# Kernel optimization log

Hardware: AMD Instinct MI355X
Metric: run time of the kernel (lower is better)

Reference implementation:

```python
import jax, jax.numpy as jnp
import numpy as np

B, S, D, H, L, DFF, NA = 128, 52, 1024, 16, 8, 4096, 1000
DK = D // H
KTOP = int((1.0 - 0.9) * S)  # per-row top-k kept before threshold = 5
EPS = 1e-5
SCALE = 1.0 / np.sqrt(DK).astype(np.float32)


def setup_inputs() -> dict:
    key = jax.random.key(0)
    ks = jax.random.split(key, 30)
    # token grid: channels 0,1 in [0,50) so only designated positions match special tokens
    x = jax.random.randint(ks[0], (B, S, 3), 0, 50).astype(jnp.int32)
    act = jax.random.randint(ks[1], (B, S), 0, NA).astype(jnp.int32)
    x = x.at[..., 2].set(act)
    x = x.at[:, 0].set(jnp.array([100, 0, 1], jnp.int32))    # SOS
    x = x.at[:, 26].set(jnp.array([100, 0, 2], jnp.int32))   # SEP
    x = x.at[:, 48:].set(jnp.array([100, 0, 0], jnp.int32))  # PAD tail

    def n(k, shape, scale=0.02):
        return (jax.random.normal(k, shape) * scale).astype(jnp.float32)

    return dict(
        x=x,
        action_emb=n(ks[2], (NA, D), 1.0),
        sep_token=n(ks[3], (D,), 1.0),
        bn_gamma=jnp.ones((S,), jnp.float32),
        bn_beta=jnp.zeros((S,), jnp.float32),
        Wq=n(ks[4], (L, D, D)), bq=jnp.zeros((L, D), jnp.float32),
        Wk=n(ks[5], (L, D, D)), bk=jnp.zeros((L, D), jnp.float32),
        Wv=n(ks[6], (L, D, D)), bv=jnp.zeros((L, D), jnp.float32),
        Wo=n(ks[7], (L, D, D)), bo=jnp.zeros((L, D), jnp.float32),
        W1=n(ks[8], (L, DFF, D)), b1=jnp.zeros((L, DFF), jnp.float32),
        W2=n(ks[9], (L, D, DFF)), b2=jnp.zeros((L, D), jnp.float32),
        ln1_g=jnp.ones((L, D), jnp.float32), ln1_b=jnp.zeros((L, D), jnp.float32),
        ln2_g=jnp.ones((L, D), jnp.float32), ln2_b=jnp.zeros((L, D), jnp.float32),
        Wout=n(ks[10], (3, D)), bout=jnp.zeros((3,), jnp.float32),
    )


def _ln(x, g, b):
    m = x.mean(-1, keepdims=True)
    v = x.var(-1, keepdims=True)
    return (x - m) * jax.lax.rsqrt(v + EPS) * g + b


def reference(x, action_emb, sep_token, bn_gamma, bn_beta,
              Wq, bq, Wk, bk, Wv, bv, Wo, bo,
              W1, b1, W2, b2, ln1_g, ln1_b, ln2_g, ln2_b, Wout, bout):
    PAD = jnp.array([100, 0, 0], x.dtype)
    SEP = jnp.array([100, 0, 2], x.dtype)
    pad = jnp.all(x == PAD, -1)            # [B,S]
    sep = jnp.all(x == SEP, -1)            # [B,S]
    valid = ~pad                            # attend only to non-pad keys

    # token-scatter embedding: sep positions -> sep_token, everything else -> action embedding
    h = jnp.where(sep[..., None], sep_token, action_emb[x[..., 2]])  # [B,S,D]

    # BatchNorm1d(52) over seq-as-channel dim (training-mode batch stats)
    mu = h.mean((0, 2), keepdims=True)
    var = h.var((0, 2), keepdims=True)
    h = (h - mu) * jax.lax.rsqrt(var + EPS) * bn_gamma[None, :, None] + bn_beta[None, :, None]

    for l in range(L):
        q = (h @ Wq[l].T + bq[l]).reshape(B, S, H, DK).transpose(0, 2, 1, 3)
        k = (h @ Wk[l].T + bk[l]).reshape(B, S, H, DK).transpose(0, 2, 1, 3)
        v = (h @ Wv[l].T + bv[l]).reshape(B, S, H, DK).transpose(0, 2, 1, 3)
        scores = jnp.einsum('bhqd,bhkd->bhqk', q, k) * SCALE       # [B,H,S,S]
        scores = jnp.where(valid[:, None, None, :], scores, -1e9)
        thr = jax.lax.top_k(scores, KTOP)[0][..., -1:]              # per-row k-th largest
        sparse = scores * (scores >= thr).astype(scores.dtype)      # zero out sub-threshold
        attn = jax.nn.softmax(sparse, axis=-1)
        o = jnp.einsum('bhqk,bhkd->bhqd', attn, v).transpose(0, 2, 1, 3).reshape(B, S, D)
        o = o @ Wo[l].T + bo[l]
        h = _ln(h + o, ln1_g[l], ln1_b[l])
        f = jax.nn.relu(h @ W1[l].T + b1[l]) @ W2[l].T + b2[l]
        h = _ln(h + f, ln2_g[l], ln2_b[l])

    y = h @ Wout.T + bout                                           # [B,S,3]
    return y[:, -1]
```

## Files before the change

kernel.cpp:

```cpp
#include <hip/hip_runtime.h>
#include <cstddef>
#include <cstdint>

#define B_    128
#define S_    52
#define D_    1024
#define H_    16
#define L_    8
#define DFF_  4096
#define DK_   64
#define T_    (B_*S_)
#define EPS_  1e-5f
#define SCALE_ 0.125f

typedef unsigned short ushortx4 __attribute__((ext_vector_type(4)));
typedef short  bf16x8 __attribute__((ext_vector_type(8)));
typedef float  f32x4  __attribute__((ext_vector_type(4)));

__device__ __forceinline__ unsigned short f2b(float f) {
  unsigned int u = __builtin_bit_cast(unsigned int, f);
  u = u + 0x7fffu + ((u >> 16) & 1u);
  return (unsigned short)(u >> 16);
}
__device__ __forceinline__ float b2f(unsigned short b) {
  unsigned int u = ((unsigned int)b) << 16;
  return __builtin_bit_cast(float, u);
}
__device__ __forceinline__ void gload16(const void* g, void* l) {
  __builtin_amdgcn_global_load_lds((const __attribute__((address_space(1))) unsigned int*)g,
      (__attribute__((address_space(3))) unsigned int*)l, 16, 0, 0);
}

__global__ __launch_bounds__(256) void k_embed(const int* __restrict__ x,
    const float* __restrict__ aemb, const float* __restrict__ sept,
    float* __restrict__ h, float* __restrict__ part, int* __restrict__ mask)
{
  int row = blockIdx.x;
  int b = row / S_;
  int s = row - b * S_;
  const int* xr = x + (size_t)row * 3;
  int x0 = xr[0], x1 = xr[1], x2 = xr[2];
  bool issep = (x0 == 100) && (x1 == 0) && (x2 == 2);
  bool ispad = (x0 == 100) && (x1 == 0) && (x2 == 0);
  int t = threadIdx.x;
  if (t == 0) mask[row] = ispad ? 0 : 1;
  const float* src = issep ? sept : (aemb + (size_t)x2 * D_);
  size_t base = (size_t)row * D_;
  float s1 = 0.f, s2 = 0.f;
#pragma unroll
  for (int i = 0; i < 4; ++i) {
    int d = t + i * 256;
    float v = src[d];
    h[base + d] = v;
    s1 += v;
    s2 += v * v;
  }
#pragma unroll
  for (int off = 32; off; off >>= 1) {
    s1 += __shfl_down(s1, off);
    s2 += __shfl_down(s2, off);
  }
  __shared__ float red[8];
  int lane = t & 63, wid = t >> 6;
  if (lane == 0) { red[wid] = s1; red[4 + wid] = s2; }
  __syncthreads();
  if (t == 0) {
    part[(size_t)s * B_ + b]        = red[0] + red[1] + red[2] + red[3];
    part[(size_t)(S_ + s) * B_ + b] = red[4] + red[5] + red[6] + red[7];
  }
}

__global__ __launch_bounds__(128) void k_bn_reduce(const float* __restrict__ part,
                                                   float* __restrict__ stats)
{
  int s = blockIdx.x;
  int t = threadIdx.x;
  float s1 = part[(size_t)s * B_ + t];
  float s2 = part[(size_t)(S_ + s) * B_ + t];
#pragma unroll
  for (int off = 32; off; off >>= 1) {
    s1 += __shfl_down(s1, off);
    s2 += __shfl_down(s2, off);
  }
  __shared__ float red[4];
  int lane = t & 63, wid = t >> 6;
  if (lane == 0) { red[wid] = s1; red[2 + wid] = s2; }
  __syncthreads();
  if (t == 0) {
    stats[s]      = red[0] + red[1];
    stats[S_ + s] = red[2] + red[3];
  }
}

__global__ __launch_bounds__(256) void k_bn_apply(float* __restrict__ h,
    const float* __restrict__ stats, const float* __restrict__ g,
    const float* __restrict__ bb, unsigned short* __restrict__ hb)
{
  int row = blockIdx.x;
  int s = row % S_;
  const float cnt = (float)(B_ * D_);
  float mu  = stats[s] / cnt;
  float var = stats[S_ + s] / cnt - mu * mu;
  float sc  = rsqrtf(var + EPS_) * g[s];
  float off = bb[s] - mu * sc;
  size_t base = (size_t)row * D_;
  int t = threadIdx.x;
#pragma unroll
  for (int i = 0; i < 4; ++i) {
    int d = t + i * 256;
    float v = h[base + d] * sc + off;
    h[base + d] = v;
    hb[base + d] = f2b(v);
  }
}

__global__ __launch_bounds__(256) void k_wconv(
    const float* __restrict__ wq, const float* __restrict__ wk,
    const float* __restrict__ wv, const float* __restrict__ wo,
    const float* __restrict__ w1, const float* __restrict__ w2,
    unsigned short* __restrict__ out)
{
  const size_t DD = (size_t)D_ * D_;
  const size_t DF = (size_t)DFF_ * D_;
  const size_t total = 4 * DD + 2 * DF;
  size_t stride = (size_t)gridDim.x * 256 * 4;
  for (size_t i = ((size_t)blockIdx.x * 256 + threadIdx.x) * 4; i < total; i += stride) {
    const float* src; size_t off;
    if      (i < DD)          { src = wq; off = i; }
    else if (i < 2 * DD)      { src = wk; off = i - DD; }
    else if (i < 3 * DD)      { src = wv; off = i - 2 * DD; }
    else if (i < 4 * DD)      { src = wo; off = i - 3 * DD; }
    else if (i < 4 * DD + DF) { src = w1; off = i - 4 * DD; }
    else                      { src = w2; off = i - 4 * DD - DF; }
    float4 v = *reinterpret_cast<const float4*>(src + off);
    ushortx4 o = { f2b(v.x), f2b(v.y), f2b(v.z), f2b(v.w) };
    *reinterpret_cast<ushortx4*>(out + i) = o;
  }
}

__global__ __launch_bounds__(256) void k_bcat(const float* __restrict__ bq,
    const float* __restrict__ bk, const float* __restrict__ bv,
    float* __restrict__ out)
{
  int i = blockIdx.x * 256 + threadIdx.x;
  int l = i / 3072, j = i - l * 3072;
  float v = (j < D_) ? bq[l * D_ + j] : (j < 2 * D_) ? bk[l * D_ + j - D_]
                                                     : bv[l * D_ + j - 2 * D_];
  out[i] = v;
}

__global__ void k_zero32(int* __restrict__ cnt) { cnt[threadIdx.x] = 0; }

template<int RELU, int OUTBF16>
__global__ __launch_bounds__(512, 4) void k_gemm_p(
    const unsigned short* __restrict__ A, const unsigned short* __restrict__ Wt,
    const float* __restrict__ bias, void* __restrict__ C0, void* __restrict__ C1,
    int Mtiles, int Ntiles, int parts, int K, int ldc, int* __restrict__ cnt)
{
  __shared__ unsigned short lds[3 * 12288];
  __shared__ int sTile;
  const int tid = threadIdx.x;
  const int w = tid >> 6, l = tid & 63;

  const int tpp = Mtiles * Ntiles;
  const int nwg = tpp * parts;
  const int KH = K / parts;
  const int NT = KH >> 5;

  const int colsw = 16 * ((l & 3) ^ ((l >> 3) & 3));
  const size_t r16 = (size_t)16 * K * 2;
  unsigned short* lA = lds + w * 1024;
  unsigned short* lB = lds + 8192 + w * 512;
  const int fr = l & 15, kg = l >> 4;
  const int wr = w >> 1, wc = w & 1;
  const int xk = 16 * (kg ^ ((fr >> 1) & 3));
  const int aOff = (wr * 64 + fr) * 64 + xk;
  const int bOff = 16384 + (wc * 64 + fr) * 64 + xk;

  for (;;) {
    if (tid == 0) sTile = atomicAdd(cnt, 1);
    __syncthreads();
    const int tl = sTile;
    if (tl >= nwg) break;
    const int part = tl / tpp;
    const int rem  = tl - part * tpp;
    const int bxn  = rem % Ntiles;
    const int bym  = rem / Ntiles;
    const int bm = bym * 256, bn = bxn * 128;

    const char* gA = (const char*)A + ((size_t)(bm + w * 32 + (l >> 2)) * K + (size_t)part * KH) * 2 + colsw;
    const char* gB = (const char*)Wt + ((size_t)(bn + w * 16 + (l >> 2)) * K + (size_t)part * KH) * 2 + colsw;

#define STAGE(tt, bb) do {                          \
    size_t ko_ = (size_t)(tt) * 64;                 \
    unsigned short* la_ = lA + (bb) * 12288;        \
    unsigned short* lb_ = lB + (bb) * 12288;        \
    gload16(gA + ko_,       la_);                   \
    gload16(gA + ko_ + r16, la_ + 512);             \
    gload16(gB + ko_,       lb_);                   \
  } while (0)

    f32x4 acc[4][4] = {};
    STAGE(0, 0);
    STAGE(1, 1);
    int cur = 0;
    for (int t = 0; t < NT; ++t) {
      if (t + 1 < NT) { asm volatile("s_waitcnt vmcnt(3)" ::: "memory"); }
      else            { asm volatile("s_waitcnt vmcnt(0)" ::: "memory"); }
      __builtin_amdgcn_sched_barrier(0);
      __builtin_amdgcn_s_barrier();
      __builtin_amdgcn_sched_barrier(0);
      if (t + 2 < NT) {
        int nb = cur + 2; if (nb >= 3) nb -= 3;
        STAGE(t + 2, nb);
      }
      const char* bp = (const char*)lds + cur * 24576;
      bf16x8 af[4], bfv[4];
#pragma unroll
      for (int mf = 0; mf < 4; ++mf)
        af[mf] = *(const bf16x8*)(bp + aOff + mf * 1024);
#pragma unroll
      for (int nf = 0; nf < 4; ++nf)
        bfv[nf] = *(const bf16x8*)(bp + bOff + nf * 1024);
      asm volatile("s_waitcnt lgkmcnt(0)" ::: "memory");
      __builtin_amdgcn_sched_barrier(0);
      __builtin_amdgcn_s_setprio(1);
#pragma unroll
      for (int mf = 0; mf < 4; ++mf)
#pragma unroll
        for (int nf = 0; nf < 4; ++nf)
          acc[mf][nf] = __builtin_amdgcn_mfma_f32_16x16x32_bf16(af[mf], bfv[nf], acc[mf][nf], 0, 0, 0);
      __builtin_amdgcn_s_setprio(0);
      __builtin_amdgcn_sched_barrier(0);
      cur = (cur == 2) ? 0 : cur + 1;
    }
#undef STAGE

    void* C = part ? C1 : C0;
#pragma unroll
    for (int nf = 0; nf < 4; ++nf) {
      int col = bn + wc * 64 + nf * 16 + fr;
      float bv = (part == 0) ? bias[col] : 0.f;
#pragma unroll
      for (int mf = 0; mf < 4; ++mf) {
        int row0 = bm + wr * 64 + mf * 16 + kg * 4;
#pragma unroll
        for (int j = 0; j < 4; ++j) {
          float v = acc[mf][nf][j] + bv;
          if (RELU) v = fmaxf(v, 0.f);
          if (OUTBF16)
            ((unsigned short*)C)[(size_t)(row0 + j) * ldc + col] = f2b(v);
          else
            ((float*)C)[(size_t)(row0 + j) * ldc + col] = v;
        }
      }
    }
  }
}

__global__ __launch_bounds__(64) void k_attn(const unsigned short* __restrict__ qkv,
    const int* __restrict__ mask, unsigned short* __restrict__ ao)
{
  __shared__ float sc[64][68];
  __shared__ unsigned short ph[64][68];
  __shared__ unsigned short plo[64][68];
  __shared__ unsigned short vT[64][68];
  __shared__ float dnm[64];

  int blk = blockIdx.x;
  int b = blk >> 4, hh = blk & 15;
  int l = threadIdx.x;
  int cl = l & 15, kg = l >> 4;
  const unsigned short* base = qkv + (size_t)(b * S_) * 3072 + hh * 64;

  {
    const unsigned short* vp = base + 2048 + l;
#pragma unroll 4
    for (int k = 0; k < S_; ++k)
      vT[l][k] = vp[(size_t)k * 3072];
#pragma unroll
    for (int k = S_; k < 64; ++k) vT[l][k] = 0;
  }

  bf16x8 qa[4][2], kb[4][2];
#pragma unroll
  for (int mi = 0; mi < 4; ++mi) {
    int row = mi * 16 + cl;
    bool ok = (row < S_);
    const unsigned short* qp = base + (size_t)row * 3072 + kg * 8;
#pragma unroll
    for (int ks = 0; ks < 2; ++ks) {
      bf16x8 z = {};
      qa[mi][ks] = ok ? *reinterpret_cast<const bf16x8*>(qp + ks * 32) : z;
      kb[mi][ks] = ok ? *reinterpret_cast<const bf16x8*>(qp + 1024 + ks * 32) : z;
    }
  }

  f32x4 acc[4][4] = {};
#pragma unroll
  for (int ks = 0; ks < 2; ++ks)
#pragma unroll
    for (int mi = 0; mi < 4; ++mi)
#pragma unroll
      for (int ci = 0; ci < 4; ++ci)
        acc[mi][ci] = __builtin_amdgcn_mfma_f32_16x16x32_bf16(qa[mi][ks], kb[ci][ks], acc[mi][ci], 0, 0, 0);

  int vld[4];
#pragma unroll
  for (int ci = 0; ci < 4; ++ci) {
    int col = ci * 16 + cl;
    vld[ci] = (col < S_) ? mask[b * S_ + col] : 0;
  }
#pragma unroll
  for (int mi = 0; mi < 4; ++mi)
#pragma unroll
    for (int ci = 0; ci < 4; ++ci)
#pragma unroll
      for (int j = 0; j < 4; ++j)
        sc[mi * 16 + kg * 4 + j][ci * 16 + cl] = vld[ci] ? acc[mi][ci][j] * SCALE_ : -1e9f;

  __syncthreads();

  if (l < S_) {
    float v0 = -3e38f, v1 = -3e38f, v2 = -3e38f, v3 = -3e38f, v4 = -3e38f;
    const float4* rp = reinterpret_cast<const float4*>(&sc[l][0]);
#pragma unroll
    for (int c4 = 0; c4 < 13; ++c4) {
      float4 x = rp[c4];
      float xs[4] = { x.x, x.y, x.z, x.w };
#pragma unroll
      for (int u = 0; u < 4; ++u) {
        float xv = xs[u];
        if      (xv > v0) { v4 = v3; v3 = v2; v2 = v1; v1 = v0; v0 = xv; }
        else if (xv > v1) { v4 = v3; v3 = v2; v2 = v1; v1 = xv; }
        else if (xv > v2) { v4 = v3; v3 = v2; v2 = xv; }
        else if (xv > v3) { v4 = v3; v3 = xv; }
        else if (xv > v4) { v4 = xv; }
      }
    }
    float thr = v4;
    float m = fmaxf(v0, 0.f);
    float denom = 0.f;
    for (int c = 0; c < S_; ++c) {
      float xv = sc[l][c];
      float sp = (xv >= thr) ? xv : 0.f;
      float e = __expf(sp - m);
      denom += e;
      unsigned short hi = f2b(e);
      ph[l][c] = hi;
      plo[l][c] = f2b(e - b2f(hi));
    }
#pragma unroll
    for (int c = S_; c < 64; ++c) { ph[l][c] = 0; plo[l][c] = 0; }
    dnm[l] = 1.f / denom;
  }
  __syncthreads();

  f32x4 o[4][4] = {};
#pragma unroll
  for (int ks = 0; ks < 2; ++ks) {
    bf16x8 vf[4];
#pragma unroll
    for (int di = 0; di < 4; ++di)
      vf[di] = *reinterpret_cast<const bf16x8*>(&vT[di * 16 + cl][ks * 32 + kg * 8]);
#pragma unroll
    for (int mi = 0; mi < 4; ++mi) {
      bf16x8 ahi = *reinterpret_cast<const bf16x8*>(&ph[mi * 16 + cl][ks * 32 + kg * 8]);
      bf16x8 alo = *reinterpret_cast<const bf16x8*>(&plo[mi * 16 + cl][ks * 32 + kg * 8]);
#pragma unroll
      for (int di = 0; di < 4; ++di) {
        o[mi][di] = __builtin_amdgcn_mfma_f32_16x16x32_bf16(ahi, vf[di], o[mi][di], 0, 0, 0);
        o[mi][di] = __builtin_amdgcn_mfma_f32_16x16x32_bf16(alo, vf[di], o[mi][di], 0, 0, 0);
      }
    }
  }

#pragma unroll
  for (int mi = 0; mi < 4; ++mi) {
    int row = mi * 16 + kg * 4;
    if (row < S_) {
#pragma unroll
      for (int j = 0; j < 4; ++j) {
        int r = row + j;
        float inv = dnm[r];
        unsigned short* aop = ao + (size_t)(b * S_ + r) * D_ + hh * DK_;
#pragma unroll
        for (int di = 0; di < 4; ++di)
          aop[di * 16 + cl] = f2b(o[mi][di][j] * inv);
      }
    }
  }
}

__global__ __launch_bounds__(256) void k_add_ln(float* __restrict__ h,
    const float* __restrict__ r0, const float* __restrict__ r1,
    const float* __restrict__ g, const float* __restrict__ bb,
    unsigned short* __restrict__ hb)
{
  int row = blockIdx.x;
  size_t base = (size_t)row * D_;
  int t = threadIdx.x;
  float xs[4];
  float s1 = 0.f, s2 = 0.f;
#pragma unroll
  for (int i = 0; i < 4; ++i) {
    int d = t + i * 256;
    float xv = h[base + d] + r0[base + d] + r1[base + d];
    xs[i] = xv;
    s1 += xv;
    s2 += xv * xv;
  }
#pragma unroll
  for (int off = 32; off; off >>= 1) {
    s1 += __shfl_down(s1, off);
    s2 += __shfl_down(s2, off);
  }
  __shared__ float red[8];
  int lane = t & 63, wid = t >> 6;
  if (lane == 0) { red[wid] = s1; red[4 + wid] = s2; }
  __syncthreads();
  if (t == 0) {
    red[0] = red[0] + red[1] + red[2] + red[3];
    red[4] = red[4] + red[5] + red[6] + red[7];
  }
  __syncthreads();
  float mean = red[0] / (float)D_;
  float var  = red[4] / (float)D_ - mean * mean;
  float inv  = rsqrtf(var + EPS_);
#pragma unroll
  for (int i = 0; i < 4; ++i) {
    int d = t + i * 256;
    float v = (xs[i] - mean) * inv * g[d] + bb[d];
    h[base + d] = v;
    hb[base + d] = f2b(v);
  }
}

__global__ __launch_bounds__(256) void k_final(const float* __restrict__ h,
    const float* __restrict__ Wout, const float* __restrict__ bout,
    float* __restrict__ y)
{
  int b = blockIdx.x;
  const float* hr = h + (size_t)(b * S_ + (S_ - 1)) * D_;
  int t = threadIdx.x;
  float p0 = 0.f, p1 = 0.f, p2 = 0.f;
  for (int d = t; d < D_; d += 256) {
    float xv = hr[d];
    p0 += xv * Wout[d];
    p1 += xv * Wout[D_ + d];
    p2 += xv * Wout[2 * D_ + d];
  }
#pragma unroll
  for (int off = 32; off; off >>= 1) {
    p0 += __shfl_down(p0, off);
    p1 += __shfl_down(p1, off);
    p2 += __shfl_down(p2, off);
  }
  __shared__ float red[12];
  int lane = t & 63, wid = t >> 6;
  if (lane == 0) { red[wid] = p0; red[4 + wid] = p1; red[8 + wid] = p2; }
  __syncthreads();
  if (t == 0) {
    y[b * 3 + 0] = red[0] + red[1] + red[2]  + red[3]  + bout[0];
    y[b * 3 + 1] = red[4] + red[5] + red[6]  + red[7]  + bout[1];
    y[b * 3 + 2] = red[8] + red[9] + red[10] + red[11] + bout[2];
  }
}

extern "C" void kernel_launch(void* const* d_in, const int* in_sizes, int n_in,
                              void* d_out, int out_size, void* d_ws, size_t ws_size,
                              hipStream_t stream)
{
  const int*   x    = (const int*)d_in[0];
  const float* aemb = (const float*)d_in[1];
  const float* sept = (const float*)d_in[2];
  const float* bng  = (const float*)d_in[3];
  const float* bnb  = (const float*)d_in[4];
  const float* Wq = (const float*)d_in[5];  const float* bq = (const float*)d_in[6];
  const float* Wk = (const float*)d_in[7];  const float* bk = (const float*)d_in[8];
  const float* Wv = (const float*)d_in[9];  const float* bv = (const float*)d_in[10];
  const float* Wo = (const float*)d_in[11]; const float* bo = (const float*)d_in[12];
  const float* W1 = (const float*)d_in[13]; const float* b1 = (const float*)d_in[14];
  const float* W2 = (const float*)d_in[15]; const float* b2 = (const float*)d_in[16];
  const float* ln1g = (const float*)d_in[17]; const float* ln1b = (const float*)d_in[18];
  const float* ln2g = (const float*)d_in[19]; const float* ln2b = (const float*)d_in[20];
  const float* Wout = (const float*)d_in[21]; const float* bout = (const float*)d_in[22];
  float* out = (float*)d_out;

  float* ws = (float*)d_ws;
  const size_t TD = (size_t)T_ * D_;
  const size_t DD = (size_t)D_ * D_;
  const size_t DF = (size_t)DFF_ * D_;
  float* h   = ws;
  float* tmp = ws + TD;
  unsigned short* hb   = (unsigned short*)(ws + 2 * TD);
  unsigned short* qkvb = (unsigned short*)(ws + 2 * TD + TD / 2);
  unsigned short* aob  = (unsigned short*)(ws + 4 * TD);
  unsigned short* ffb  = (unsigned short*)(ws + 4 * TD + TD / 2);
  unsigned short* wbuf = (unsigned short*)(ws + 6 * TD + TD / 2);
  float* Pff = ws + 4 * TD + TD / 2;
  float* Pqk = ws + 2 * TD + TD / 2;
  float* bqkv = ws + 6 * TD + TD / 2 + (4 * DD + 2 * DF) / 2;
  float* stats = bqkv + L_ * 3072;
  float* part  = stats + 2 * S_;
  int*   mask  = (int*)(part + 2 * S_ * B_);
  int*   cnt   = mask + T_;

  k_zero32<<<1, 32, 0, stream>>>(cnt);
  k_embed<<<T_, 256, 0, stream>>>(x, aemb, sept, h, part, mask);
  k_bn_reduce<<<S_, 128, 0, stream>>>(part, stats);
  k_bn_apply<<<T_, 256, 0, stream>>>(h, stats, bng, bnb, hb);
  k_bcat<<<(L_ * 3072) / 256, 256, 0, stream>>>(bq, bk, bv, bqkv);

  for (int l = 0; l < L_; ++l) {
    k_wconv<<<3072, 256, 0, stream>>>(Wq + l * DD, Wk + l * DD, Wv + l * DD,
                                      Wo + l * DD, W1 + l * DF, W2 + l * DF, wbuf);
    k_gemm_p<0, 1><<<512, 512, 0, stream>>>(hb, wbuf, bqkv + l * 3072,
        qkvb, qkvb, 26, 24, 1, 1024, 3072, cnt + l * 4 + 0);
    k_attn<<<B_ * H_, 64, 0, stream>>>(qkvb, mask, aob);
    k_gemm_p<0, 0><<<416, 512, 0, stream>>>(aob, wbuf + 3 * DD, bo + l * D_,
        tmp, Pff, 26, 8, 2, 1024, 1024, cnt + l * 4 + 1);
    k_add_ln<<<T_, 256, 0, stream>>>(h, tmp, Pff, ln1g + l * D_, ln1b + l * D_, hb);
    k_gemm_p<1, 1><<<512, 512, 0, stream>>>(hb, wbuf + 4 * DD, b1 + l * DFF_,
        ffb, ffb, 26, 32, 1, 1024, 4096, cnt + l * 4 + 2);
    k_gemm_p<0, 0><<<416, 512, 0, stream>>>(ffb, wbuf + 4 * DD + DF, b2 + l * D_,
        tmp, Pqk, 26, 8, 2, 4096, 1024, cnt + l * 4 + 3);
    k_add_ln<<<T_, 256, 0, stream>>>(h, tmp, Pqk, ln2g + l * D_, ln2b + l * D_, hb);
  }
  k_final<<<B_, 256, 0, stream>>>(h, Wout, bout, out);
}
```

Before: 2.771 ms.

## Replace persistent atomic-scheduled GEMM with 128x128 tiles and half-stage pipeline

Replaces the persistent GEMM, which fetched 256x128 tiles through an atomic counter with 512 threads, with a one-tile-per-block 128x128 kernel using 256 threads and an XCD-style block-index swizzle. The K loop now streams each K-step in two half-stages across a 5-slot LDS ring and splits the MFMA work into two halves with a barrier between them, so loads overlap more finely with compute. The counter-zeroing kernel and atomics go away. In exchange each block does less work, there are more launches' worth of blocks and more barriers per K-step, and the B tile gets reloaded more often.

Measured after the change: 2.765 ms. Within noise of the previous version (-0.2%).

```diff
diff --git a/kernel.cpp b/kernel.cpp
--- a/kernel.cpp
+++ b/kernel.cpp
@@ -149,110 +149,117 @@
   out[i] = v;
 }
 
-__global__ void k_zero32(int* __restrict__ cnt) { cnt[threadIdx.x] = 0; }
-
 template<int RELU, int OUTBF16>
-__global__ __launch_bounds__(512, 4) void k_gemm_p(
+__global__ __launch_bounds__(256, 4) void k_gemm5(
     const unsigned short* __restrict__ A, const unsigned short* __restrict__ Wt,
     const float* __restrict__ bias, void* __restrict__ C0, void* __restrict__ C1,
-    int Mtiles, int Ntiles, int parts, int K, int ldc, int* __restrict__ cnt)
-{
-  __shared__ unsigned short lds[3 * 12288];
-  __shared__ int sTile;
+    int Mtiles, int Ntiles, int parts, int K, int ldc)
+{
+  __shared__ char lds[5 * 8192];
   const int tid = threadIdx.x;
   const int w = tid >> 6, l = tid & 63;
 
   const int tpp = Mtiles * Ntiles;
   const int nwg = tpp * parts;
+  int id = blockIdx.x;
+  int swz = (id & 7) * (nwg >> 3) + (id >> 3);
+  const int part = swz / tpp;
+  const int rem = swz - part * tpp;
+  const int bym = rem / Ntiles;
+  const int bxn = rem - bym * Ntiles;
+  const int bm = bym * 128, bn = bxn * 128;
   const int KH = K / parts;
   const int NT = KH >> 5;
 
-  const int colsw = 16 * ((l & 3) ^ ((l >> 3) & 3));
-  const size_t r16 = (size_t)16 * K * 2;
-  unsigned short* lA = lds + w * 1024;
-  unsigned short* lB = lds + 8192 + w * 512;
+  const int colsw = 16 * ((tid & 3) ^ ((tid >> 3) & 3));
+  const char* gA = (const char*)A + ((size_t)(bm + (tid >> 2)) * K + (size_t)part * KH) * 2 + colsw;
+  const char* gB = (const char*)Wt + ((size_t)(bn + (tid >> 2)) * K + (size_t)part * KH) * 2 + colsw;
+  const size_t rP = (size_t)64 * K * 2;
+  const int ldsW = w * 1024;
+
   const int fr = l & 15, kg = l >> 4;
   const int wr = w >> 1, wc = w & 1;
   const int xk = 16 * (kg ^ ((fr >> 1) & 3));
-  const int aOff = (wr * 64 + fr) * 64 + xk;
-  const int bOff = 16384 + (wc * 64 + fr) * 64 + xk;
-
-  for (;;) {
-    if (tid == 0) sTile = atomicAdd(cnt, 1);
-    __syncthreads();
-    const int tl = sTile;
-    if (tl >= nwg) break;
-    const int part = tl / tpp;
-    const int rem  = tl - part * tpp;
-    const int bxn  = rem % Ntiles;
-    const int bym  = rem / Ntiles;
-    const int bm = bym * 256, bn = bxn * 128;
-
-    const char* gA = (const char*)A + ((size_t)(bm + w * 32 + (l >> 2)) * K + (size_t)part * KH) * 2 + colsw;
-    const char* gB = (const char*)Wt + ((size_t)(bn + w * 16 + (l >> 2)) * K + (size_t)part * KH) * 2 + colsw;
-
-#define STAGE(tt, bb) do {                          \
-    size_t ko_ = (size_t)(tt) * 64;                 \
-    unsigned short* la_ = lA + (bb) * 12288;        \
-    unsigned short* lb_ = lB + (bb) * 12288;        \
-    gload16(gA + ko_,       la_);                   \
-    gload16(gA + ko_ + r16, la_ + 512);             \
-    gload16(gB + ko_,       lb_);                   \
+  const int aBase = fr * 64 + xk;
+  const int bBase = 4096 + fr * 64 + xk;
+
+  f32x4 acc[4][4] = {};
+  int sA = wr, sB = wc, s4 = 4, s5 = 0;
+
+#define STAGEH(tt, pp, ss) do {                                     \
+    size_t ko_ = (size_t)(tt) * 64 + (size_t)(pp) * rP;             \
+    gload16(gA + ko_, lds + (ss) * 8192 + ldsW);                    \
+    gload16(gB + ko_, lds + (ss) * 8192 + 4096 + ldsW);             \
   } while (0)
 
-    f32x4 acc[4][4] = {};
-    STAGE(0, 0);
-    STAGE(1, 1);
-    int cur = 0;
-    for (int t = 0; t < NT; ++t) {
-      if (t + 1 < NT) { asm volatile("s_waitcnt vmcnt(3)" ::: "memory"); }
-      else            { asm volatile("s_waitcnt vmcnt(0)" ::: "memory"); }
-      __builtin_amdgcn_sched_barrier(0);
-      __builtin_amdgcn_s_barrier();
-      __builtin_amdgcn_sched_barrier(0);
-      if (t + 2 < NT) {
-        int nb = cur + 2; if (nb >= 3) nb -= 3;
-        STAGE(t + 2, nb);
-      }
-      const char* bp = (const char*)lds + cur * 24576;
-      bf16x8 af[4], bfv[4];
-#pragma unroll
-      for (int mf = 0; mf < 4; ++mf)
-        af[mf] = *(const bf16x8*)(bp + aOff + mf * 1024);
-#pragma unroll
-      for (int nf = 0; nf < 4; ++nf)
-        bfv[nf] = *(const bf16x8*)(bp + bOff + nf * 1024);
-      asm volatile("s_waitcnt lgkmcnt(0)" ::: "memory");
-      __builtin_amdgcn_sched_barrier(0);
-      __builtin_amdgcn_s_setprio(1);
-#pragma unroll
-      for (int mf = 0; mf < 4; ++mf)
-#pragma unroll
-        for (int nf = 0; nf < 4; ++nf)
-          acc[mf][nf] = __builtin_amdgcn_mfma_f32_16x16x32_bf16(af[mf], bfv[nf], acc[mf][nf], 0, 0, 0);
-      __builtin_amdgcn_s_setprio(0);
-      __builtin_amdgcn_sched_barrier(0);
-      cur = (cur == 2) ? 0 : cur + 1;
-    }
-#undef STAGE
-
-    void* C = part ? C1 : C0;
-#pragma unroll
-    for (int nf = 0; nf < 4; ++nf) {
-      int col = bn + wc * 64 + nf * 16 + fr;
-      float bv = (part == 0) ? bias[col] : 0.f;
-#pragma unroll
-      for (int mf = 0; mf < 4; ++mf) {
-        int row0 = bm + wr * 64 + mf * 16 + kg * 4;
-#pragma unroll
-        for (int j = 0; j < 4; ++j) {
-          float v = acc[mf][nf][j] + bv;
-          if (RELU) v = fmaxf(v, 0.f);
-          if (OUTBF16)
-            ((unsigned short*)C)[(size_t)(row0 + j) * ldc + col] = f2b(v);
-          else
-            ((float*)C)[(size_t)(row0 + j) * ldc + col] = v;
-        }
+  STAGEH(0, 0, 0);
+  STAGEH(0, 1, 1);
+  STAGEH(1, 0, 2);
+  STAGEH(1, 1, 3);
+  asm volatile("s_waitcnt vmcnt(4)" ::: "memory");
+  __builtin_amdgcn_sched_barrier(0);
+
+  for (int t = 0; t < NT; ++t) {
+    const bool st = (t + 2 < NT);
+    if (st) STAGEH(t + 2, 0, s4);
+    __builtin_amdgcn_sched_barrier(0);
+    __builtin_amdgcn_s_barrier();
+    __builtin_amdgcn_sched_barrier(0);
+    const char* pa = lds + sA * 8192 + aBase;
+    const char* pb = lds + sB * 8192 + bBase;
+    bf16x8 af[4], bfv[4];
+#pragma unroll
+    for (int mf = 0; mf < 4; ++mf) af[mf] = *(const bf16x8*)(pa + mf * 1024);
+#pragma unroll
+    for (int nf = 0; nf < 4; ++nf) bfv[nf] = *(const bf16x8*)(pb + nf * 1024);
+    asm volatile("s_waitcnt lgkmcnt(0)" ::: "memory");
+    __builtin_amdgcn_sched_barrier(0);
+    __builtin_amdgcn_s_setprio(1);
+#pragma unroll
+    for (int mf = 0; mf < 4; ++mf) {
+      acc[mf][0] = __builtin_amdgcn_mfma_f32_16x16x32_bf16(af[mf], bfv[0], acc[mf][0], 0, 0, 0);
+      acc[mf][1] = __builtin_amdgcn_mfma_f32_16x16x32_bf16(af[mf], bfv[1], acc[mf][1], 0, 0, 0);
+    }
+    __builtin_amdgcn_s_setprio(0);
+    __builtin_amdgcn_sched_barrier(0);
+    __builtin_amdgcn_s_barrier();
+    __builtin_amdgcn_sched_barrier(0);
+    if (st) STAGEH(t + 2, 1, s5);
+    __builtin_amdgcn_sched_barrier(0);
+    __builtin_amdgcn_s_setprio(1);
+#pragma unroll
+    for (int mf = 0; mf < 4; ++mf) {
+      acc[mf][2] = __builtin_amdgcn_mfma_f32_16x16x32_bf16(af[mf], bfv[2], acc[mf][2], 0, 0, 0);
+      acc[mf][3] = __builtin_amdgcn_mfma_f32_16x16x32_bf16(af[mf], bfv[3], acc[mf][3], 0, 0, 0);
+    }
+    __builtin_amdgcn_s_setprio(0);
+    __builtin_amdgcn_sched_barrier(0);
+    if (st) { asm volatile("s_waitcnt vmcnt(4)" ::: "memory"); }
+    else    { asm volatile("s_waitcnt vmcnt(0)" ::: "memory"); }
+    __builtin_amdgcn_sched_barrier(0);
+    sA += 2; if (sA >= 5) sA -= 5;
+    sB += 2; if (sB >= 5) sB -= 5;
+    s4 += 2; if (s4 >= 5) s4 -= 5;
+    s5 += 2; if (s5 >= 5) s5 -= 5;
+  }
+#undef STAGEH
+
+  void* C = part ? C1 : C0;
+#pragma unroll
+  for (int nf = 0; nf < 4; ++nf) {
+    int col = bn + wc * 64 + nf * 16 + fr;
+    float bv = (part == 0) ? bias[col] : 0.f;
+#pragma unroll
+    for (int mf = 0; mf < 4; ++mf) {
+      int row0 = bm + wr * 64 + mf * 16 + kg * 4;
+#pragma unroll
+      for (int j = 0; j < 4; ++j) {
+        float v = acc[mf][nf][j] + bv;
+        if (RELU) v = fmaxf(v, 0.f);
+        if (OUTBF16)
+          ((unsigned short*)C)[(size_t)(row0 + j) * ldc + col] = f2b(v);
+        else
+          ((float*)C)[(size_t)(row0 + j) * ldc + col] = v;
       }
     }
   }
@@ -504,9 +511,7 @@
   float* stats = bqkv + L_ * 3072;
   float* part  = stats + 2 * S_;
   int*   mask  = (int*)(part + 2 * S_ * B_);
-  int*   cnt   = mask + T_;
-
-  k_zero32<<<1, 32, 0, stream>>>(cnt);
+
   k_embed<<<T_, 256, 0, stream>>>(x, aemb, sept, h, part, mask);
   k_bn_reduce<<<S_, 128, 0, stream>>>(part, stats);
   k_bn_apply<<<T_, 256, 0, stream>>>(h, stats, bng, bnb, hb);
@@ -515,16 +520,16 @@
   for (int l = 0; l < L_; ++l) {
     k_wconv<<<3072, 256, 0, stream>>>(Wq + l * DD, Wk + l * DD, Wv + l * DD,
                                       Wo + l * DD, W1 + l * DF, W2 + l * DF, wbuf);
-    k_gemm_p<0, 1><<<512, 512, 0, stream>>>(hb, wbuf, bqkv + l * 3072,
-        qkvb, qkvb, 26, 24, 1, 1024, 3072, cnt + l * 4 + 0);
+    k_gemm5<0, 1><<<52 * 24, 256, 0, stream>>>(hb, wbuf, bqkv + l * 3072,
+        qkvb, qkvb, 52, 24, 1, 1024, 3072);
     k_attn<<<B_ * H_, 64, 0, stream>>>(qkvb, mask, aob);
-    k_gemm_p<0, 0><<<416, 512, 0, stream>>>(aob, wbuf + 3 * DD, bo + l * D_,
-        tmp, Pff, 26, 8, 2, 1024, 1024, cnt + l * 4 + 1);
+    k_gemm5<0, 0><<<832, 256, 0, stream>>>(aob, wbuf + 3 * DD, bo + l * D_,
+        tmp, Pff, 52, 8, 2, 1024, 1024);
     k_add_ln<<<T_, 256, 0, stream>>>(h, tmp, Pff, ln1g + l * D_, ln1b + l * D_, hb);
-    k_gemm_p<1, 1><<<512, 512, 0, stream>>>(hb, wbuf + 4 * DD, b1 + l * DFF_,
-        ffb, ffb, 26, 32, 1, 1024, 4096, cnt + l * 4 + 2);
-    k_gemm_p<0, 0><<<416, 512, 0, stream>>>(ffb, wbuf + 4 * DD + DF, b2 + l * D_,
-        tmp, Pqk, 26, 8, 2, 4096, 1024, cnt + l * 4 + 3);
+    k_gemm5<1, 1><<<52 * 32, 256, 0, stream>>>(hb, wbuf + 4 * DD, b1 + l * DFF_,
+        ffb, ffb, 52, 32, 1, 1024, 4096);
+    k_gemm5<0, 0><<<832, 256, 0, stream>>>(ffb, wbuf + 4 * DD + DF, b2 + l * D_,
+        tmp, Pqk, 52, 8, 2, 4096, 1024);
     k_add_ln<<<T_, 256, 0, stream>>>(h, tmp, Pqk, ln2g + l * D_, ln2b + l * D_, hb);
   }
   k_final<<<B_, 256, 0, stream>>>(h, Wout, bout, out);
```
